# Performance work log

Hardware: AMD Instinct MI355X
Metric: run time of the kernel (lower is better)

## Reference

```python
import jax, jax.numpy as jnp
import numpy as np

DIM, E, K, H = 512, 8, 2, 16  # hidden_dim is hardcoded to 16 in the torch module
B, N = 8, 4096
BN_EPS = 1e-5


def setup_inputs() -> dict:
    key = jax.random.key(0)
    ks = jax.random.split(key, 12)
    s = 0.02
    return {
        "x": jax.random.normal(ks[0], (B, N, DIM), jnp.float32),
        # gate: Conv1d(dim, dim, 1) -> weight [dim, dim]; BatchNorm1d(dim); Conv1d(dim, E, 1)
        "wg1": jax.random.normal(ks[1], (DIM, DIM), jnp.float32) * s,
        "bg1": jnp.zeros((DIM,), jnp.float32),
        "gamma": jnp.ones((DIM,), jnp.float32),
        "beta": jnp.zeros((DIM,), jnp.float32),
        "wg2": jax.random.normal(ks[2], (E, DIM), jnp.float32) * s,
        "bg2": jnp.zeros((E,), jnp.float32),
        # experts stacked: Linear(dim,16) -> w1 [E, dim, 16]; Linear(16,dim) -> w2 [E, 16, dim]
        "w1": jax.random.normal(ks[3], (E, DIM, H), jnp.float32) * s,
        "b1": jnp.zeros((E, H), jnp.float32),
        "w2": jax.random.normal(ks[4], (E, H, DIM), jnp.float32) * s,
        "b2": jnp.zeros((E, DIM), jnp.float32),
    }


def reference(x, wg1, bg1, gamma, beta, wg2, bg2, w1, b1, w2, b2):
    b, n, c = x.shape
    t = b * n
    flat = x.reshape(t, c)                                 # [T, C]

    # gate: 1x1 conv == per-token linear; BN over all tokens per channel (train-mode batch stats)
    h = flat @ wg1.T + bg1                                  # [T, C]
    mu = h.mean(axis=0)
    var = h.var(axis=0)                                     # biased, matches torch BN normalization
    h = gamma * (h - mu) * jax.lax.rsqrt(var + BN_EPS) + beta
    h = jax.nn.relu(h)
    logits = h @ wg2.T + bg2                                # [T, E]

    vals, idx = jax.lax.top_k(logits, K)                    # [T, K]
    topk_w = jax.nn.softmax(vals, axis=-1)
    weight = jnp.zeros((t, logits.shape[-1]), logits.dtype)
    weight = weight.at[jnp.arange(t)[:, None], idx].set(topk_w)  # scatter, [T, E]

    # dense expert compute for every token (faithful to original)
    h1 = jax.nn.relu(jnp.einsum('tc,ech->teh', flat, w1) + b1)   # [T, E, H]
    all_out = jnp.einsum('teh,ehc->tec', h1, w2) + b2            # [T, E, C]
    out_flat = jnp.einsum('tec,te->tc', all_out, weight)         # masked combine

    out = out_flat.reshape(b, n, c).transpose(0, 2, 1)           # [B, C, N]
    usage = weight.sum(axis=0) / t
    lb_loss = (usage ** 2).sum() * logits.shape[-1]
    return out, lb_loss
```

## Files before the change

### kernel.cpp

```cpp
#include <hip/hip_runtime.h>

#define T_TOK 32768
#define C_DIM 512
#define N_SEQ 4096

typedef unsigned short ushort_t;
typedef unsigned int uint_t;
typedef __attribute__((ext_vector_type(8))) _Float16 half8;
typedef __attribute__((ext_vector_type(4))) float f32x4;

static __device__ __forceinline__ ushort_t f2h_bits(float f) {
  _Float16 h = (_Float16)f;
  return __builtin_bit_cast(ushort_t, h);
}
static __device__ __forceinline__ float h_bits2f(ushort_t u) {
  return (float)__builtin_bit_cast(_Float16, u);
}

static __device__ __forceinline__ half8 frag_ld(const ushort_t* base, int r, int q) {
  const int off = r * 32 + ((q ^ ((r >> 1) & 3)) * 8);
  return *(const half8*)(base + off);
}

#define GLOAD_LDS(gptr, lptr)                                                  \
  __builtin_amdgcn_global_load_lds(                                            \
      (const __attribute__((address_space(1))) uint_t*)(gptr),                 \
      (__attribute__((address_space(3))) uint_t*)(lptr), 16, 0, 0)

__global__ __launch_bounds__(256) void prep(
    const float* __restrict__ X, const float* __restrict__ wg1,
    const float* __restrict__ w1, const float* __restrict__ w2,
    const float* __restrict__ b2, ushort_t* __restrict__ Ahi,
    ushort_t* __restrict__ Alo, ushort_t* __restrict__ Whi,
    ushort_t* __restrict__ Wlo, ushort_t* __restrict__ W1t,
    ushort_t* __restrict__ W2t, float* __restrict__ stats,
    float* __restrict__ usage) {
  const int idx = blockIdx.x * 256 + threadIdx.x;
  {
    const size_t i0 = (size_t)idx * 8;
    float4 a = *(const float4*)(X + i0);
    float4 b = *(const float4*)(X + i0 + 4);
    float v[8] = {a.x, a.y, a.z, a.w, b.x, b.y, b.z, b.w};
    ushort_t hi[8], lo[8];
#pragma unroll
    for (int j = 0; j < 8; ++j) {
      hi[j] = f2h_bits(v[j]);
      lo[j] = f2h_bits(v[j] - h_bits2f(hi[j]));
    }
    *(uint4*)(Ahi + i0) = *(uint4*)hi;
    *(uint4*)(Alo + i0) = *(uint4*)lo;
  }
  if (blockIdx.x < 1024) {
    {
      const float v = wg1[idx];
      const ushort_t h = f2h_bits(v);
      Whi[idx] = h;
      Wlo[idx] = f2h_bits(v - h_bits2f(h));
    }
    if (idx < 65536) {
      const int eh = idx >> 9, c = idx & 511;
      const int e = eh >> 4, hh = eh & 15;
      W1t[idx] = f2h_bits(w1[((size_t)e * 512 + c) * 16 + hh]);
    }
    if (idx < 81920) {
      const int c = idx / 160, k = idx - c * 160;
      float v = 0.f;
      if (k < 128) {
        const int e = k >> 4, hh = k & 15;
        v = w2[((size_t)e * 16 + hh) * 512 + c];
      } else if (k < 136) {
        v = b2[(size_t)(k - 128) * 512 + c];
      }
      W2t[c * 160 + k] = f2h_bits(v);
    }
  }
  if (blockIdx.x == 4096) {
    float4 z = {0.f, 0.f, 0.f, 0.f};
    *(float4*)&stats[threadIdx.x * 4] = z;
    if (threadIdx.x < 8) usage[threadIdx.x] = 0.f;
  }
}

__global__ __launch_bounds__(256) void k1_mfma(
    const ushort_t* __restrict__ Ahi, const ushort_t* __restrict__ Alo,
    const ushort_t* __restrict__ Whi, const ushort_t* __restrict__ Wlo,
    const float* __restrict__ bg1, float* __restrict__ H,
    float* __restrict__ stats) {
  __shared__ ushort_t sAh[4096], sAl[4096], sBh[4096], sBl[4096];
  const int tid = threadIdx.x, lane = tid & 63, w = tid >> 6;
  const int wm = w >> 1, wn = w & 1;
  const int m0 = blockIdx.y * 128, n0 = blockIdx.x * 128;

  const ushort_t* gsrc;
  ushort_t* lbase;
  int rowbase;
  if (w == 0)      { gsrc = Ahi; lbase = sAh; rowbase = m0; }
  else if (w == 1) { gsrc = Alo; lbase = sAl; rowbase = m0; }
  else if (w == 2) { gsrc = Whi; lbase = sBh; rowbase = n0; }
  else             { gsrc = Wlo; lbase = sBl; rowbase = n0; }

  f32x4 acc[4][4] = {};
  const int cl = lane & 15, qf = lane >> 4;

  for (int kc = 0; kc < 16; ++kc) {
    const int k0 = kc * 32;
    __syncthreads();
#pragma unroll
    for (int j = 0; j < 8; ++j) {
      const int p = j * 64 + lane;
      const int r = p >> 2, q = (p & 3) ^ ((r >> 1) & 3);
      GLOAD_LDS(gsrc + (size_t)(rowbase + r) * 512 + k0 + q * 8, lbase + j * 512);
    }
    __syncthreads();
    half8 ah[4], al[4], bh[4], bl[4];
#pragma unroll
    for (int f = 0; f < 4; ++f) {
      ah[f] = frag_ld(sAh, wm * 64 + f * 16 + cl, qf);
      al[f] = frag_ld(sAl, wm * 64 + f * 16 + cl, qf);
      bh[f] = frag_ld(sBh, wn * 64 + f * 16 + cl, qf);
      bl[f] = frag_ld(sBl, wn * 64 + f * 16 + cl, qf);
    }
#pragma unroll
    for (int i = 0; i < 4; ++i)
#pragma unroll
      for (int j = 0; j < 4; ++j) {
        acc[i][j] = __builtin_amdgcn_mfma_f32_16x16x32_f16(ah[i], bh[j], acc[i][j], 0, 0, 0);
        acc[i][j] = __builtin_amdgcn_mfma_f32_16x16x32_f16(ah[i], bl[j], acc[i][j], 0, 0, 0);
        acc[i][j] = __builtin_amdgcn_mfma_f32_16x16x32_f16(al[i], bh[j], acc[i][j], 0, 0, 0);
      }
  }

  float s[4] = {0, 0, 0, 0}, qs[4] = {0, 0, 0, 0};
  const int rq = lane >> 4;
#pragma unroll
  for (int nf = 0; nf < 4; ++nf) {
    const int col = n0 + wn * 64 + nf * 16 + cl;
    const float bv = bg1[col];
#pragma unroll
    for (int mf = 0; mf < 4; ++mf) {
      const int row = m0 + wm * 64 + mf * 16 + rq * 4;
#pragma unroll
      for (int i = 0; i < 4; ++i) {
        const float v = acc[mf][nf][i] + bv;
        H[(size_t)(row + i) * 512 + col] = v;
        s[nf] += v;
        qs[nf] += v * v;
      }
    }
  }
#pragma unroll
  for (int nf = 0; nf < 4; ++nf) {
    s[nf] += __shfl_xor(s[nf], 16, 64);
    qs[nf] += __shfl_xor(qs[nf], 16, 64);
    s[nf] += __shfl_xor(s[nf], 32, 64);
    qs[nf] += __shfl_xor(qs[nf], 32, 64);
  }
  if (lane < 16) {
#pragma unroll
    for (int nf = 0; nf < 4; ++nf) {
      const int col = n0 + wn * 64 + nf * 16 + cl;
      atomicAdd(&stats[col], s[nf]);
      atomicAdd(&stats[512 + col], qs[nf]);
    }
  }
}

__global__ __launch_bounds__(256) void k4_gate(
    const float* __restrict__ H, const float* __restrict__ stats,
    const float* __restrict__ gamma, const float* __restrict__ beta,
    const float* __restrict__ wg2, const float* __restrict__ bg2,
    int* __restrict__ selE, float* __restrict__ selW,
    float* __restrict__ usage) {
  __shared__ float scsh_l[1024];
  __shared__ float lus[8];
  if (threadIdx.x < 8) lus[threadIdx.x] = 0.f;
#pragma unroll
  for (int rep = 0; rep < 2; ++rep) {
    const int c = threadIdx.x + rep * 256;
    const double mu = (double)stats[c] * (1.0 / (double)T_TOK);
    const double var = (double)stats[512 + c] * (1.0 / (double)T_TOK) - mu * mu;
    const double rstd = 1.0 / sqrt(var + 1e-5);
    const float scv = (float)((double)gamma[c] * rstd);
    scsh_l[c] = scv;
    scsh_l[512 + c] = beta[c] - (float)mu * scv;
  }
  __syncthreads();

  const int wv = threadIdx.x >> 6, lane = threadIdx.x & 63;
  const int cb = lane * 8;

  float sc[8], sh[8];
#pragma unroll
  for (int i = 0; i < 8; ++i) {
    sc[i] = scsh_l[cb + i];
    sh[i] = scsh_l[512 + cb + i];
  }
  float wg[8][8];
#pragma unroll
  for (int e = 0; e < 8; ++e)
#pragma unroll
    for (int i = 0; i < 8; ++i) wg[e][i] = wg2[e * C_DIM + cb + i];
  float bg[8];
#pragma unroll
  for (int e = 0; e < 8; ++e) bg[e] = bg2[e];

  for (int it = 0; it < 16; ++it) {
    const int t = blockIdx.x * 64 + wv * 16 + it;
    const float* hr = H + (size_t)t * C_DIM + cb;
    float4 h0 = *(const float4*)hr;
    float4 h1 = *(const float4*)(hr + 4);
    float y[8] = {h0.x, h0.y, h0.z, h0.w, h1.x, h1.y, h1.z, h1.w};
#pragma unroll
    for (int i = 0; i < 8; ++i) y[i] = fmaxf(fmaf(y[i], sc[i], sh[i]), 0.f);

    float lg[8];
#pragma unroll
    for (int e = 0; e < 8; ++e) {
      float sum = 0.f;
#pragma unroll
      for (int i = 0; i < 8; ++i) sum = fmaf(y[i], wg[e][i], sum);
      lg[e] = sum;
    }
#pragma unroll
    for (int d = 1; d < 64; d <<= 1)
#pragma unroll
      for (int e = 0; e < 8; ++e) lg[e] += __shfl_xor(lg[e], d, 64);
#pragma unroll
    for (int e = 0; e < 8; ++e) lg[e] += bg[e];

    float v1 = lg[0]; int i1 = 0;
#pragma unroll
    for (int e = 1; e < 8; ++e)
      if (lg[e] > v1) { v1 = lg[e]; i1 = e; }
    float v2 = -3.4e38f; int i2 = 0;
#pragma unroll
    for (int e = 0; e < 8; ++e)
      if (e != i1 && lg[e] > v2) { v2 = lg[e]; i2 = e; }

    const float p = expf(v2 - v1);
    const float rw = 1.f / (1.f + p);
    const float w0 = rw, w1 = p * rw;

    if (lane == 0) {
      selE[2 * t] = i1;
      selE[2 * t + 1] = i2;
      selW[2 * t] = w0;
      selW[2 * t + 1] = w1;
      atomicAdd(&lus[i1], w0);
      atomicAdd(&lus[i2], w1);
    }
  }
  __syncthreads();
  if (threadIdx.x < 8) atomicAdd(&usage[threadIdx.x], lus[threadIdx.x]);
}

__global__ __launch_bounds__(256) void k5a_fc1(
    const ushort_t* __restrict__ Ahi, const ushort_t* __restrict__ W1t,
    const float* __restrict__ b1, const int* __restrict__ selE,
    const float* __restrict__ selW, ushort_t* __restrict__ Pg) {
  __shared__ ushort_t sA[4096], sB[4096];
  __shared__ ushort_t Pl[128 * 160];
  __shared__ float wtab[128 * 8];
  const int tid = threadIdx.x, lane = tid & 63, w = tid >> 6;
  const int wm = w >> 1, wn = w & 1;
  const int t0 = blockIdx.x * 128;

#pragma unroll
  for (int i = 0; i < 4; ++i) wtab[tid * 4 + i] = 0.f;
  {
    uint4 z = {0, 0, 0, 0};
    const int row = tid >> 1, hf = tid & 1;
    *(uint4*)&Pl[row * 160 + 128 + hf * 16] = z;
    *(uint4*)&Pl[row * 160 + 136 + hf * 16] = z;
  }
  __syncthreads();
  {
    const int t = tid >> 1, s = tid & 1;
    const int e = selE[(size_t)(t0 + t) * 2 + s];
    const float wv = selW[(size_t)(t0 + t) * 2 + s];
    wtab[t * 8 + e] = wv;
    Pl[t * 160 + 128 + e] = f2h_bits(wv);
  }

  f32x4 acc[4][4] = {};
  const int cl = lane & 15, qf = lane >> 4;
  for (int kc = 0; kc < 16; ++kc) {
    const int k0 = kc * 32;
    __syncthreads();
    const ushort_t* gs = (w < 2) ? Ahi : W1t;
    ushort_t* lb = (w < 2) ? sA : sB;
    const int rbase = (w < 2) ? t0 : 0;
    const int wh = w & 1;
#pragma unroll
    for (int j = 0; j < 4; ++j) {
      const int p = wh * 256 + j * 64 + lane;
      const int r = p >> 2, q = (p & 3) ^ ((r >> 1) & 3);
      GLOAD_LDS(gs + (size_t)(rbase + r) * 512 + k0 + q * 8, lb + wh * 2048 + j * 512);
    }
    __syncthreads();
    half8 af[4], bf[4];
#pragma unroll
    for (int f = 0; f < 4; ++f) {
      af[f] = frag_ld(sA, wm * 64 + f * 16 + cl, qf);
      bf[f] = frag_ld(sB, wn * 64 + f * 16 + cl, qf);
    }
#pragma unroll
    for (int i = 0; i < 4; ++i)
#pragma unroll
      for (int j = 0; j < 4; ++j)
        acc[i][j] = __builtin_amdgcn_mfma_f32_16x16x32_f16(af[i], bf[j], acc[i][j], 0, 0, 0);
  }

  {
    const int rq = lane >> 4;
#pragma unroll
    for (int nf = 0; nf < 4; ++nf) {
      const int col = wn * 64 + nf * 16 + cl;
      const float bv = b1[col];
      const int e = wn * 4 + nf;
#pragma unroll
      for (int mf = 0; mf < 4; ++mf) {
        const int row = wm * 64 + mf * 16 + rq * 4;
#pragma unroll
        for (int i = 0; i < 4; ++i) {
          const float v = fmaxf(acc[mf][nf][i] + bv, 0.f) * wtab[(row + i) * 8 + e];
          Pl[(row + i) * 160 + col] = f2h_bits(v);
        }
      }
    }
  }
  __syncthreads();
  {
    const int row = tid >> 1, half = tid & 1;
    const uint4* src = (const uint4*)&Pl[row * 160 + half * 80];
    uint4* dst = (uint4*)(Pg + (size_t)(t0 + row) * 160 + half * 80);
#pragma unroll
    for (int j = 0; j < 10; ++j) dst[j] = src[j];
  }
}

__global__ __launch_bounds__(256) void k5b_fc2(
    const ushort_t* __restrict__ Pg, const ushort_t* __restrict__ W2t,
    const float* __restrict__ usage, float* __restrict__ Out) {
  __shared__ ushort_t sA[4096], sB[4096];
  __shared__ float ys[128 * 68];
  const int tid = threadIdx.x, lane = tid & 63, w = tid >> 6;
  const int wm = w >> 1, wn = w & 1;
  const int t0 = blockIdx.x * 128;
  const int bi = t0 >> 12, n0 = t0 & 4095;
  const int cl = lane & 15, qf = lane >> 4, rq = lane >> 4;

  if (blockIdx.x == 0 && tid == 0) {
    float s = 0.f;
#pragma unroll
    for (int e = 0; e < 8; ++e) {
      const float u = usage[e] * (1.f / (float)T_TOK);
      s += u * u;
    }
    Out[(size_t)16777216] = s * 8.f;
  }

  for (int nc = 0; nc < 4; ++nc) {
    f32x4 acc[4][4] = {};
    for (int kc = 0; kc < 5; ++kc) {
      const int k0 = kc * 32;
      __syncthreads();
      const ushort_t* gs = (w < 2) ? Pg : W2t;
      ushort_t* lb = (w < 2) ? sA : sB;
      const int rbase = (w < 2) ? t0 : nc * 128;
      const int wh = w & 1;
#pragma unroll
      for (int j = 0; j < 4; ++j) {
        const int p = wh * 256 + j * 64 + lane;
        const int r = p >> 2, q = (p & 3) ^ ((r >> 1) & 3);
        GLOAD_LDS(gs + (size_t)(rbase + r) * 160 + k0 + q * 8, lb + wh * 2048 + j * 512);
      }
      __syncthreads();
      half8 af[4], bf4[4];
#pragma unroll
      for (int f = 0; f < 4; ++f) {
        af[f] = frag_ld(sA, wm * 64 + f * 16 + cl, qf);
        bf4[f] = frag_ld(sB, wn * 64 + f * 16 + cl, qf);
      }
#pragma unroll
      for (int i = 0; i < 4; ++i)
#pragma unroll
        for (int j = 0; j < 4; ++j)
          acc[i][j] = __builtin_amdgcn_mfma_f32_16x16x32_f16(af[i], bf4[j], acc[i][j], 0, 0, 0);
    }
#pragma unroll
    for (int half = 0; half < 2; ++half) {
      __syncthreads();
      if (wm == half) {
#pragma unroll
        for (int nf = 0; nf < 4; ++nf) {
          const int c = wn * 64 + nf * 16 + cl;
#pragma unroll
          for (int mf = 0; mf < 4; ++mf) {
            const int trow = mf * 16 + rq * 4;
#pragma unroll
            for (int i = 0; i < 4; ++i) ys[c * 68 + trow + i] = acc[mf][nf][i];
          }
        }
      }
      __syncthreads();
#pragma unroll
      for (int pass = 0; pass < 8; ++pass) {
        const int c = pass * 16 + (tid >> 4);
        const int f4 = tid & 15;
        float4 v = *(const float4*)&ys[c * 68 + f4 * 4];
        *(float4*)&Out[((size_t)(bi * 512 + nc * 128 + c)) * 4096 + n0 + half * 64 + f4 * 4] = v;
      }
    }
  }
}

extern "C" void kernel_launch(void* const* d_in, const int* in_sizes, int n_in,
                              void* d_out, int out_size, void* d_ws, size_t ws_size,
                              hipStream_t stream) {
  const float* x     = (const float*)d_in[0];
  const float* wg1   = (const float*)d_in[1];
  const float* bg1   = (const float*)d_in[2];
  const float* gamma = (const float*)d_in[3];
  const float* beta  = (const float*)d_in[4];
  const float* wg2   = (const float*)d_in[5];
  const float* bg2   = (const float*)d_in[6];
  const float* w1    = (const float*)d_in[7];
  const float* b1    = (const float*)d_in[8];
  const float* w2    = (const float*)d_in[9];
  const float* b2    = (const float*)d_in[10];
  float* out = (float*)d_out;

  char* ws = (char*)d_ws;
  float*    h     = (float*)ws;
  ushort_t* Ahi   = (ushort_t*)(ws + 67108864);
  ushort_t* Alo   = (ushort_t*)(ws + 100663296);
  ushort_t* Pg    = (ushort_t*)(ws + 134217728);
  ushort_t* Whi   = (ushort_t*)(ws + 144703488);
  ushort_t* Wlo   = (ushort_t*)(ws + 145227776);
  ushort_t* W1t   = (ushort_t*)(ws + 145752064);
  ushort_t* W2t   = (ushort_t*)(ws + 145883136);
  float*    stats = (float*)(ws + 146046976);
  float*    usage = (float*)(ws + 146051072);
  int*      selE  = (int*)(ws + 146051104);
  float*    selW  = (float*)(ws + 146313248);

  prep<<<8192, 256, 0, stream>>>(x, wg1, w1, w2, b2, Ahi, Alo, Whi, Wlo, W1t,
                                 W2t, stats, usage);
  k1_mfma<<<dim3(4, 256), 256, 0, stream>>>(Ahi, Alo, Whi, Wlo, bg1, h, stats);
  k4_gate<<<512, 256, 0, stream>>>(h, stats, gamma, beta, wg2, bg2, selE, selW,
                                   usage);
  k5a_fc1<<<256, 256, 0, stream>>>(Ahi, W1t, b1, selE, selW, Pg);
  k5b_fc2<<<256, 256, 0, stream>>>(Pg, W2t, usage, out);
}
```

Baseline: 272.3 us.

## Fuse gate, fc1 and fc2 into one kernel and swizzle k1 block order

Merges the gating kernel and both expert GEMM kernels into a single kernel per 128-token tile. Routing weights and the fc1 output stay in LDS instead of round-tripping through global selE/selW/Pg buffers. The load-balance loss is now computed by the last block, chosen through an atomic ticket counter. k1's grid is flattened with a swizzled block-to-tile mapping for better L2 reuse. The fused kernel uses more LDS and runs only 256 blocks, which may limit occupancy and overlap.

```diff
diff --git a/kernel.cpp b/kernel.cpp
--- a/kernel.cpp
+++ b/kernel.cpp
@@ -34,7 +34,7 @@
     ushort_t* __restrict__ Alo, ushort_t* __restrict__ Whi,
     ushort_t* __restrict__ Wlo, ushort_t* __restrict__ W1t,
     ushort_t* __restrict__ W2t, float* __restrict__ stats,
-    float* __restrict__ usage) {
+    float* __restrict__ usage, uint_t* __restrict__ done) {
   const int idx = blockIdx.x * 256 + threadIdx.x;
   {
     const size_t i0 = (size_t)idx * 8;
@@ -78,6 +78,7 @@
     float4 z = {0.f, 0.f, 0.f, 0.f};
     *(float4*)&stats[threadIdx.x * 4] = z;
     if (threadIdx.x < 8) usage[threadIdx.x] = 0.f;
+    if (threadIdx.x == 8) *done = 0u;
   }
 }
 
@@ -89,7 +90,9 @@
   __shared__ ushort_t sAh[4096], sAl[4096], sBh[4096], sBl[4096];
   const int tid = threadIdx.x, lane = tid & 63, w = tid >> 6;
   const int wm = w >> 1, wn = w & 1;
-  const int m0 = blockIdx.y * 128, n0 = blockIdx.x * 128;
+  const int b = blockIdx.x;
+  const int m0 = ((b & 7) | ((b >> 5) << 3)) * 128;
+  const int n0 = ((b >> 3) & 3) * 128;
 
   const ushort_t* gsrc;
   ushort_t* lbase;
@@ -165,18 +168,39 @@
   }
 }
 
-__global__ __launch_bounds__(256) void k4_gate(
+__global__ __launch_bounds__(256) void k5_fused(
+    const ushort_t* __restrict__ Ahi, const ushort_t* __restrict__ W1t,
+    const ushort_t* __restrict__ W2t, const float* __restrict__ b1,
     const float* __restrict__ H, const float* __restrict__ stats,
     const float* __restrict__ gamma, const float* __restrict__ beta,
     const float* __restrict__ wg2, const float* __restrict__ bg2,
-    int* __restrict__ selE, float* __restrict__ selW,
-    float* __restrict__ usage) {
+    float* __restrict__ usage, uint_t* __restrict__ done,
+    float* __restrict__ Out) {
+  __shared__ ushort_t sA[4096], sB[4096];
+  __shared__ ushort_t Pl[128 * 168];
+  __shared__ float wtab[128 * 8];
+  __shared__ float ys[128 * 68];
   __shared__ float scsh_l[1024];
   __shared__ float lus[8];
-  if (threadIdx.x < 8) lus[threadIdx.x] = 0.f;
+
+  const int tid = threadIdx.x, lane = tid & 63, w = tid >> 6;
+  const int wm = w >> 1, wn = w & 1;
+  const int t0 = blockIdx.x * 128;
+  const int bi = t0 >> 12, n0 = t0 & 4095;
+  const int cl = lane & 15, qf = lane >> 4, rq = lane >> 4;
+
+  if (tid < 8) lus[tid] = 0.f;
+#pragma unroll
+  for (int i = 0; i < 4; ++i) wtab[tid * 4 + i] = 0.f;
+  {
+    uint4 z = {0, 0, 0, 0};
+    const int row = tid >> 1, hf = tid & 1;
+    *(uint4*)&Pl[row * 168 + 128 + hf * 16] = z;
+    *(uint4*)&Pl[row * 168 + 136 + hf * 16] = z;
+  }
 #pragma unroll
   for (int rep = 0; rep < 2; ++rep) {
-    const int c = threadIdx.x + rep * 256;
+    const int c = tid + rep * 256;
     const double mu = (double)stats[c] * (1.0 / (double)T_TOK);
     const double var = (double)stats[512 + c] * (1.0 / (double)T_TOK) - mu * mu;
     const double rstd = 1.0 / sqrt(var + 1e-5);
@@ -186,104 +210,89 @@
   }
   __syncthreads();
 
-  const int wv = threadIdx.x >> 6, lane = threadIdx.x & 63;
-  const int cb = lane * 8;
-
-  float sc[8], sh[8];
-#pragma unroll
-  for (int i = 0; i < 8; ++i) {
-    sc[i] = scsh_l[cb + i];
-    sh[i] = scsh_l[512 + cb + i];
-  }
-  float wg[8][8];
-#pragma unroll
-  for (int e = 0; e < 8; ++e)
-#pragma unroll
-    for (int i = 0; i < 8; ++i) wg[e][i] = wg2[e * C_DIM + cb + i];
-  float bg[8];
-#pragma unroll
-  for (int e = 0; e < 8; ++e) bg[e] = bg2[e];
-
-  for (int it = 0; it < 16; ++it) {
-    const int t = blockIdx.x * 64 + wv * 16 + it;
-    const float* hr = H + (size_t)t * C_DIM + cb;
-    float4 h0 = *(const float4*)hr;
-    float4 h1 = *(const float4*)(hr + 4);
-    float y[8] = {h0.x, h0.y, h0.z, h0.w, h1.x, h1.y, h1.z, h1.w};
-#pragma unroll
-    for (int i = 0; i < 8; ++i) y[i] = fmaxf(fmaf(y[i], sc[i], sh[i]), 0.f);
-
-    float lg[8];
-#pragma unroll
-    for (int e = 0; e < 8; ++e) {
-      float sum = 0.f;
-#pragma unroll
-      for (int i = 0; i < 8; ++i) sum = fmaf(y[i], wg[e][i], sum);
-      lg[e] = sum;
-    }
-#pragma unroll
-    for (int d = 1; d < 64; d <<= 1)
-#pragma unroll
-      for (int e = 0; e < 8; ++e) lg[e] += __shfl_xor(lg[e], d, 64);
-#pragma unroll
-    for (int e = 0; e < 8; ++e) lg[e] += bg[e];
-
-    float v1 = lg[0]; int i1 = 0;
-#pragma unroll
-    for (int e = 1; e < 8; ++e)
-      if (lg[e] > v1) { v1 = lg[e]; i1 = e; }
-    float v2 = -3.4e38f; int i2 = 0;
+  {
+    const int cb = lane * 8;
+    float sc[8], sh[8];
+#pragma unroll
+    for (int i = 0; i < 8; ++i) {
+      sc[i] = scsh_l[cb + i];
+      sh[i] = scsh_l[512 + cb + i];
+    }
+    float wg[8][8];
 #pragma unroll
     for (int e = 0; e < 8; ++e)
-      if (e != i1 && lg[e] > v2) { v2 = lg[e]; i2 = e; }
-
-    const float p = expf(v2 - v1);
-    const float rw = 1.f / (1.f + p);
-    const float w0 = rw, w1 = p * rw;
-
-    if (lane == 0) {
-      selE[2 * t] = i1;
-      selE[2 * t + 1] = i2;
-      selW[2 * t] = w0;
-      selW[2 * t + 1] = w1;
-      atomicAdd(&lus[i1], w0);
-      atomicAdd(&lus[i2], w1);
+#pragma unroll
+      for (int i = 0; i < 8; ++i) wg[e][i] = wg2[e * C_DIM + cb + i];
+    float bg[8];
+#pragma unroll
+    for (int e = 0; e < 8; ++e) bg[e] = bg2[e];
+
+#pragma unroll 2
+    for (int it = 0; it < 32; ++it) {
+      const int tl = w * 32 + it;
+      const float* hr = H + (size_t)(t0 + tl) * C_DIM + cb;
+      float4 h0 = *(const float4*)hr;
+      float4 h1 = *(const float4*)(hr + 4);
+      float y[8] = {h0.x, h0.y, h0.z, h0.w, h1.x, h1.y, h1.z, h1.w};
+#pragma unroll
+      for (int i = 0; i < 8; ++i) y[i] = fmaxf(fmaf(y[i], sc[i], sh[i]), 0.f);
+
+      float lg[8];
+#pragma unroll
+      for (int e = 0; e < 8; ++e) {
+        float sum = 0.f;
+#pragma unroll
+        for (int i = 0; i < 8; ++i) sum = fmaf(y[i], wg[e][i], sum);
+        lg[e] = sum;
+      }
+#pragma unroll
+      for (int d = 1; d < 64; d <<= 1)
+#pragma unroll
+        for (int e = 0; e < 8; ++e) lg[e] += __shfl_xor(lg[e], d, 64);
+#pragma unroll
+      for (int e = 0; e < 8; ++e) lg[e] += bg[e];
+
+      float v1 = lg[0]; int i1 = 0;
+#pragma unroll
+      for (int e = 1; e < 8; ++e)
+        if (lg[e] > v1) { v1 = lg[e]; i1 = e; }
+      float v2 = -3.4e38f; int i2 = 0;
+#pragma unroll
+      for (int e = 0; e < 8; ++e)
+        if (e != i1 && lg[e] > v2) { v2 = lg[e]; i2 = e; }
+
+      const float p = expf(v2 - v1);
+      const float rw = 1.f / (1.f + p);
+      const float w0 = rw, w1 = p * rw;
+
+      if (lane == 0) {
+        wtab[tl * 8 + i1] = w0;
+        wtab[tl * 8 + i2] = w1;
+        Pl[tl * 168 + 128 + i1] = f2h_bits(w0);
+        Pl[tl * 168 + 128 + i2] = f2h_bits(w1);
+        atomicAdd(&lus[i1], w0);
+        atomicAdd(&lus[i2], w1);
+      }
     }
   }
   __syncthreads();
-  if (threadIdx.x < 8) atomicAdd(&usage[threadIdx.x], lus[threadIdx.x]);
-}
-
-__global__ __launch_bounds__(256) void k5a_fc1(
-    const ushort_t* __restrict__ Ahi, const ushort_t* __restrict__ W1t,
-    const float* __restrict__ b1, const int* __restrict__ selE,
-    const float* __restrict__ selW, ushort_t* __restrict__ Pg) {
-  __shared__ ushort_t sA[4096], sB[4096];
-  __shared__ ushort_t Pl[128 * 160];
-  __shared__ float wtab[128 * 8];
-  const int tid = threadIdx.x, lane = tid & 63, w = tid >> 6;
-  const int wm = w >> 1, wn = w & 1;
-  const int t0 = blockIdx.x * 128;
-
-#pragma unroll
-  for (int i = 0; i < 4; ++i) wtab[tid * 4 + i] = 0.f;
-  {
-    uint4 z = {0, 0, 0, 0};
-    const int row = tid >> 1, hf = tid & 1;
-    *(uint4*)&Pl[row * 160 + 128 + hf * 16] = z;
-    *(uint4*)&Pl[row * 160 + 136 + hf * 16] = z;
-  }
+  if (tid < 8) atomicAdd(&usage[tid], lus[tid]);
   __syncthreads();
-  {
-    const int t = tid >> 1, s = tid & 1;
-    const int e = selE[(size_t)(t0 + t) * 2 + s];
-    const float wv = selW[(size_t)(t0 + t) * 2 + s];
-    wtab[t * 8 + e] = wv;
-    Pl[t * 160 + 128 + e] = f2h_bits(wv);
+  if (tid == 0) {
+    __threadfence();
+    const uint_t ticket = atomicAdd(done, 1u);
+    if (ticket == 255u) {
+      float s = 0.f;
+#pragma unroll
+      for (int e = 0; e < 8; ++e) {
+        const float u = atomicAdd(&usage[e], 0.f) * (1.f / (float)T_TOK);
+        s += u * u;
+      }
+      Out[(size_t)16777216] = s * 8.f;
+    }
   }
 
   f32x4 acc[4][4] = {};
-  const int cl = lane & 15, qf = lane >> 4;
   for (int kc = 0; kc < 16; ++kc) {
     const int k0 = kc * 32;
     __syncthreads();
@@ -312,7 +321,6 @@
   }
 
   {
-    const int rq = lane >> 4;
 #pragma unroll
     for (int nf = 0; nf < 4; ++nf) {
       const int col = wn * 64 + nf * 16 + cl;
@@ -324,69 +332,35 @@
 #pragma unroll
         for (int i = 0; i < 4; ++i) {
           const float v = fmaxf(acc[mf][nf][i] + bv, 0.f) * wtab[(row + i) * 8 + e];
-          Pl[(row + i) * 160 + col] = f2h_bits(v);
+          Pl[(row + i) * 168 + col] = f2h_bits(v);
         }
       }
     }
   }
-  __syncthreads();
-  {
-    const int row = tid >> 1, half = tid & 1;
-    const uint4* src = (const uint4*)&Pl[row * 160 + half * 80];
-    uint4* dst = (uint4*)(Pg + (size_t)(t0 + row) * 160 + half * 80);
-#pragma unroll
-    for (int j = 0; j < 10; ++j) dst[j] = src[j];
-  }
-}
-
-__global__ __launch_bounds__(256) void k5b_fc2(
-    const ushort_t* __restrict__ Pg, const ushort_t* __restrict__ W2t,
-    const float* __restrict__ usage, float* __restrict__ Out) {
-  __shared__ ushort_t sA[4096], sB[4096];
-  __shared__ float ys[128 * 68];
-  const int tid = threadIdx.x, lane = tid & 63, w = tid >> 6;
-  const int wm = w >> 1, wn = w & 1;
-  const int t0 = blockIdx.x * 128;
-  const int bi = t0 >> 12, n0 = t0 & 4095;
-  const int cl = lane & 15, qf = lane >> 4, rq = lane >> 4;
-
-  if (blockIdx.x == 0 && tid == 0) {
-    float s = 0.f;
-#pragma unroll
-    for (int e = 0; e < 8; ++e) {
-      const float u = usage[e] * (1.f / (float)T_TOK);
-      s += u * u;
-    }
-    Out[(size_t)16777216] = s * 8.f;
-  }
 
   for (int nc = 0; nc < 4; ++nc) {
-    f32x4 acc[4][4] = {};
+    f32x4 a2[4][4] = {};
     for (int kc = 0; kc < 5; ++kc) {
       const int k0 = kc * 32;
       __syncthreads();
-      const ushort_t* gs = (w < 2) ? Pg : W2t;
-      ushort_t* lb = (w < 2) ? sA : sB;
-      const int rbase = (w < 2) ? t0 : nc * 128;
-      const int wh = w & 1;
-#pragma unroll
-      for (int j = 0; j < 4; ++j) {
-        const int p = wh * 256 + j * 64 + lane;
+#pragma unroll
+      for (int j = 0; j < 2; ++j) {
+        const int p = w * 128 + j * 64 + lane;
         const int r = p >> 2, q = (p & 3) ^ ((r >> 1) & 3);
-        GLOAD_LDS(gs + (size_t)(rbase + r) * 160 + k0 + q * 8, lb + wh * 2048 + j * 512);
+        GLOAD_LDS(W2t + (size_t)(nc * 128 + r) * 160 + k0 + q * 8, sB + w * 1024 + j * 512);
       }
       __syncthreads();
       half8 af[4], bf4[4];
 #pragma unroll
       for (int f = 0; f < 4; ++f) {
-        af[f] = frag_ld(sA, wm * 64 + f * 16 + cl, qf);
+        af[f] = *(const half8*)(Pl + (wm * 64 + f * 16 + cl) * 168 + k0 + qf * 8);
         bf4[f] = frag_ld(sB, wn * 64 + f * 16 + cl, qf);
       }
 #pragma unroll
       for (int i = 0; i < 4; ++i)
 #pragma unroll
         for (int j = 0; j < 4; ++j)
-          acc[i][j] = __builtin_amdgcn_mfma_f32_16x16x32_f16(af[i], bf4[j], acc[i][j], 0, 0, 0);
+          a2[i][j] = __builtin_amdgcn_mfma_f32_16x16x32_f16(af[i], bf4[j], a2[i][j], 0, 0, 0);
     }
 #pragma unroll
     for (int half = 0; half < 2; ++half) {
@@ -399,7 +373,7 @@
           for (int mf = 0; mf < 4; ++mf) {
             const int trow = mf * 16 + rq * 4;
 #pragma unroll
-            for (int i = 0; i < 4; ++i) ys[c * 68 + trow + i] = acc[mf][nf][i];
+            for (int i = 0; i < 4; ++i) ys[c * 68 + trow + i] = a2[mf][nf][i];
           }
         }
       }
@@ -435,21 +409,17 @@
   float*    h     = (float*)ws;
   ushort_t* Ahi   = (ushort_t*)(ws + 67108864);
   ushort_t* Alo   = (ushort_t*)(ws + 100663296);
-  ushort_t* Pg    = (ushort_t*)(ws + 134217728);
-  ushort_t* Whi   = (ushort_t*)(ws + 144703488);
-  ushort_t* Wlo   = (ushort_t*)(ws + 145227776);
-  ushort_t* W1t   = (ushort_t*)(ws + 145752064);
-  ushort_t* W2t   = (ushort_t*)(ws + 145883136);
-  float*    stats = (float*)(ws + 146046976);
-  float*    usage = (float*)(ws + 146051072);
-  int*      selE  = (int*)(ws + 146051104);
-  float*    selW  = (float*)(ws + 146313248);
+  ushort_t* Whi   = (ushort_t*)(ws + 134217728);
+  ushort_t* Wlo   = (ushort_t*)(ws + 134742016);
+  ushort_t* W1t   = (ushort_t*)(ws + 135266304);
+  ushort_t* W2t   = (ushort_t*)(ws + 135397376);
+  float*    stats = (float*)(ws + 135561216);
+  float*    usage = (float*)(ws + 135565312);
+  uint_t*   done  = (uint_t*)(ws + 135565344);
 
   prep<<<8192, 256, 0, stream>>>(x, wg1, w1, w2, b2, Ahi, Alo, Whi, Wlo, W1t,
-                                 W2t, stats, usage);
-  k1_mfma<<<dim3(4, 256), 256, 0, stream>>>(Ahi, Alo, Whi, Wlo, bg1, h, stats);
-  k4_gate<<<512, 256, 0, stream>>>(h, stats, gamma, beta, wg2, bg2, selE, selW,
-                                   usage);
-  k5a_fc1<<<256, 256, 0, stream>>>(Ahi, W1t, b1, selE, selW, Pg);
-  k5b_fc2<<<256, 256, 0, stream>>>(Pg, W2t, usage, out);
-}
+                                 W2t, stats, usage, done);
+  k1_mfma<<<1024, 256, 0, stream>>>(Ahi, Alo, Whi, Wlo, bg1, h, stats);
+  k5_fused<<<256, 256, 0, stream>>>(Ahi, W1t, W2t, b1, h, stats, gamma, beta,
+                                    wg2, bg2, usage, done, out);
+}
```

After: 270.2 us. About the same (-0.8%).
